# Performance work log

Measured on AMD Instinct MI355X. Metric: run time of the kernel, lower is better.

## Reference

```python
import jax, jax.numpy as jnp
import numpy as np

T, H, E, I, TOPK = 2048, 1024, 8, 2048, 2


def setup_inputs() -> dict:
    key = jax.random.key(0)
    k1, k2, k3, k4 = jax.random.split(key, 4)
    hidden_states = jax.random.normal(k1, (T, H), dtype=jnp.float32)
    router_logits = jax.random.normal(k2, (T, E), dtype=jnp.float32)
    # w13: merged gate+up projection [E, 2I, H]; w2: down projection [E, H, I]
    w13_weight = jax.random.normal(k3, (E, 2 * I, H), dtype=jnp.float32) * 0.02
    w2_weight = jax.random.normal(k4, (E, H, I), dtype=jnp.float32) * 0.02
    return {
        "hidden_states": hidden_states,
        "router_logits": router_logits,
        "w13_weight": w13_weight,
        "w2_weight": w2_weight,
        "top_k": TOPK,
    }


def reference(hidden_states, router_logits, w13_weight, w2_weight, top_k):
    num_experts = router_logits.shape[-1]
    # --- top-k routing (softmax -> top_k -> renormalize) ---
    probs = jax.nn.softmax(router_logits, axis=-1)           # [T, E]
    topk_w, topk_ids = jax.lax.top_k(probs, top_k)           # [T, K]
    topk_w = topk_w / jnp.sum(topk_w, axis=-1, keepdims=True)
    # per-token combine weight for each expert: [T, E]
    onehot = jax.nn.one_hot(topk_ids, num_experts, dtype=hidden_states.dtype)  # [T, K, E]
    combine_w = jnp.einsum("tk,tke->te", topk_w, onehot)
    # --- grouped expert GEMMs (gated SiLU MLP) ---
    gu = jnp.einsum("th,eih->tei", hidden_states, w13_weight)  # [T, E, 2I]
    inter = w13_weight.shape[1] // 2
    gate, up = gu[..., :inter], gu[..., inter:]
    act = jax.nn.silu(gate) * up                               # [T, E, I]
    y = jnp.einsum("tei,ehi->teh", act, w2_weight)             # [T, E, H]
    # --- combine ---
    out = jnp.einsum("teh,te->th", y, combine_w)               # [T, H]
    return out
```

## Files before the change

kernel.cpp:

```cpp
#include <hip/hip_runtime.h>

#define T_ 2048
#define H_ 1024
#define E_ 8
#define I_ 2048

typedef short bf16x8 __attribute__((ext_vector_type(8)));
typedef float f32x4 __attribute__((ext_vector_type(4)));
typedef unsigned short u16x8 __attribute__((ext_vector_type(8)));

__device__ __forceinline__ unsigned short f2bf(float f) {
  unsigned u = __builtin_bit_cast(unsigned, f);
  u += 0x7fffu + ((u >> 16) & 1u);
  return (unsigned short)(u >> 16);
}

__device__ __forceinline__ float bf2f(unsigned short h) {
  unsigned u = ((unsigned)h) << 16;
  return __builtin_bit_cast(float, u);
}

#define GLOAD_LDS16(g, l)                                                     \
  __builtin_amdgcn_global_load_lds(                                           \
      (const __attribute__((address_space(1))) unsigned int*)(g),             \
      (__attribute__((address_space(3))) unsigned int*)(l), 16, 0, 0)

__global__ __launch_bounds__(256) void cvt_kernel(const float* __restrict__ s,
                                                  unsigned short* __restrict__ d,
                                                  int n8) {
  int i = blockIdx.x * blockDim.x + threadIdx.x;
  if (i >= n8) return;
  const float4* s4 = (const float4*)s;
  float4 a = s4[2 * i], b = s4[2 * i + 1];
  u16x8 v;
  v[0] = f2bf(a.x); v[1] = f2bf(a.y); v[2] = f2bf(a.z); v[3] = f2bf(a.w);
  v[4] = f2bf(b.x); v[5] = f2bf(b.y); v[6] = f2bf(b.z); v[7] = f2bf(b.w);
  *(u16x8*)(d + (size_t)i * 8) = v;
}

__global__ __launch_bounds__(256) void pack_w13(const float* __restrict__ src,
                                                unsigned short* __restrict__ dst) {
  int g = blockIdx.x * 256 + threadIdx.x;
#pragma unroll
  for (int j = 0; j < 4; ++j) {
    size_t fo = ((size_t)g * 4 + j) * 8;
    int e = (int)(fo >> 22);
    int grow = (int)((fo >> 10) & 4095);
    int col = (int)(fo & 1023);
    int nt, r;
    if (grow < 2048) { nt = grow >> 6; r = grow & 63; }
    else             { int i2 = grow - 2048; nt = i2 >> 6; r = 64 + (i2 & 63); }
    int kt = col >> 6;
    int c = (col & 63) >> 3;
    const float4* s = (const float4*)(src + fo);
    float4 a = s[0], b = s[1];
    u16x8 o;
    o[0] = f2bf(a.x); o[1] = f2bf(a.y); o[2] = f2bf(a.z); o[3] = f2bf(a.w);
    o[4] = f2bf(b.x); o[5] = f2bf(b.y); o[6] = f2bf(b.z); o[7] = f2bf(b.w);
    size_t tb = (size_t)((e * 32 + nt) * 16 + kt);
    *(u16x8*)(dst + tb * 8192 + r * 64 + ((c ^ (r & 7)) * 8)) = o;
  }
}

__global__ __launch_bounds__(256) void pack_w2(const float* __restrict__ src,
                                               unsigned short* __restrict__ dst) {
  int g = blockIdx.x * 256 + threadIdx.x;
#pragma unroll
  for (int j = 0; j < 4; ++j) {
    size_t fo = ((size_t)g * 4 + j) * 8;
    int e = (int)(fo >> 21);
    int h = (int)((fo >> 11) & 1023);
    int col = (int)(fo & 2047);
    int nt = h >> 7, r = h & 127;
    int kt = col >> 6;
    int c = (col & 63) >> 3;
    const float4* s = (const float4*)(src + fo);
    float4 a = s[0], b = s[1];
    u16x8 o;
    o[0] = f2bf(a.x); o[1] = f2bf(a.y); o[2] = f2bf(a.z); o[3] = f2bf(a.w);
    o[4] = f2bf(b.x); o[5] = f2bf(b.y); o[6] = f2bf(b.z); o[7] = f2bf(b.w);
    size_t tb = (size_t)((e * 8 + nt) * 32 + kt);
    *(u16x8*)(dst + tb * 8192 + r * 64 + ((c ^ (r & 7)) * 8)) = o;
  }
}

__global__ void router_kernel(const float* __restrict__ logits,
                              int* __restrict__ cnt,
                              int* __restrict__ plist,
                              float* __restrict__ wlist) {
  int t = blockIdx.x * blockDim.x + threadIdx.x;
  if (t >= T_) return;
  float l[E_];
#pragma unroll
  for (int e = 0; e < E_; ++e) l[e] = logits[t * E_ + e];
  int i0 = 0;
#pragma unroll
  for (int e = 1; e < E_; ++e) if (l[e] > l[i0]) i0 = e;
  int i1 = (i0 == 0) ? 1 : 0;
#pragma unroll
  for (int e = 0; e < E_; ++e) if (e != i0 && l[e] > l[i1]) i1 = e;
  float w1 = 1.f / (1.f + __expf(l[i0] - l[i1]));
  float w0 = 1.f - w1;
  int s0 = atomicAdd(&cnt[i0], 1);
  plist[i0 * T_ + s0] = 2 * t;
  wlist[i0 * T_ + s0] = w0;
  int s1 = atomicAdd(&cnt[i1], 1);
  plist[i1 * T_ + s1] = 2 * t + 1;
  wlist[i1 * T_ + s1] = w1;
}

__global__ __launch_bounds__(512, 4) void gemm1_kernel(
    const unsigned short* __restrict__ hs_bf,
    const unsigned short* __restrict__ w13p,
    const int* __restrict__ cnt, const int* __restrict__ plist,
    const float* __restrict__ wlist, unsigned short* __restrict__ act) {
  const int bid = blockIdx.x;
  const int e = bid & 7;
  const int mt = (bid >> 3) & 15;
  const int nt = bid >> 7;
  const int M = cnt[e];
  if (mt * 128 >= M) return;
  const int Mrem = M - mt * 128;
  const int n0 = nt * 64;

  __shared__ __align__(16) unsigned short As[2][128 * 64];
  __shared__ __align__(16) unsigned short Bs[2][128 * 64];

  const int tid = threadIdx.x;
  const int lane = tid & 63;
  const int wid = tid >> 6;
  const int l15 = lane & 15;
  const int q = lane >> 4;
  const int wm = (wid >> 1) * 32;
  const int wn = (wid & 1) * 32;

  const unsigned short* aSrc[2];
#pragma unroll
  for (int i = 0; i < 2; ++i) {
    int row = wid * 16 + i * 8 + (lane >> 3);
    int idx = mt * 128 + ((row < Mrem) ? row : 0);
    int p = plist[e * T_ + idx] >> 1;
    aSrc[i] = hs_bf + (size_t)p * H_ + ((lane & 7) ^ (row & 7)) * 8;
  }
  const unsigned short* bTile = w13p + (size_t)((e * 32 + nt) * 16) * 8192;

#define STAGE_G1(buf, kt)                                                     \
  do {                                                                        \
    _Pragma("unroll") for (int i = 0; i < 2; ++i)                             \
        GLOAD_LDS16(aSrc[i] + (kt) * 64, &As[buf][(wid * 16 + i * 8) * 64]);  \
    _Pragma("unroll") for (int i = 0; i < 2; ++i)                             \
        GLOAD_LDS16(bTile + (size_t)(kt) * 8192 + (wid * 2 + i) * 512 +       \
                        lane * 8,                                             \
                    &Bs[buf][(wid * 2 + i) * 512]);                           \
  } while (0)

  f32x4 accg[2][2] = {};
  f32x4 accu[2][2] = {};

  STAGE_G1(0, 0);
#pragma unroll 1
  for (int kt = 0; kt < 16; ++kt) {
    const int buf = kt & 1;
    if (kt + 1 < 16) {
      STAGE_G1(buf ^ 1, kt + 1);
      asm volatile("s_waitcnt vmcnt(4)" ::: "memory");
    } else {
      asm volatile("s_waitcnt vmcnt(0)" ::: "memory");
    }
    __builtin_amdgcn_s_barrier();
    __builtin_amdgcn_sched_barrier(0);
#pragma unroll
    for (int ks = 0; ks < 2; ++ks) {
      const int co = ((ks * 4 + q) ^ (l15 & 7)) * 8;
      bf16x8 a0 = *(const bf16x8*)&As[buf][(wm + l15) * 64 + co];
      bf16x8 a1 = *(const bf16x8*)&As[buf][(wm + 16 + l15) * 64 + co];
      bf16x8 g0 = *(const bf16x8*)&Bs[buf][(wn + l15) * 64 + co];
      bf16x8 g1 = *(const bf16x8*)&Bs[buf][(wn + 16 + l15) * 64 + co];
      bf16x8 u0 = *(const bf16x8*)&Bs[buf][(64 + wn + l15) * 64 + co];
      bf16x8 u1 = *(const bf16x8*)&Bs[buf][(64 + wn + 16 + l15) * 64 + co];
      accg[0][0] = __builtin_amdgcn_mfma_f32_16x16x32_bf16(a0, g0, accg[0][0], 0, 0, 0);
      accg[0][1] = __builtin_amdgcn_mfma_f32_16x16x32_bf16(a0, g1, accg[0][1], 0, 0, 0);
      accg[1][0] = __builtin_amdgcn_mfma_f32_16x16x32_bf16(a1, g0, accg[1][0], 0, 0, 0);
      accg[1][1] = __builtin_amdgcn_mfma_f32_16x16x32_bf16(a1, g1, accg[1][1], 0, 0, 0);
      accu[0][0] = __builtin_amdgcn_mfma_f32_16x16x32_bf16(a0, u0, accu[0][0], 0, 0, 0);
      accu[0][1] = __builtin_amdgcn_mfma_f32_16x16x32_bf16(a0, u1, accu[0][1], 0, 0, 0);
      accu[1][0] = __builtin_amdgcn_mfma_f32_16x16x32_bf16(a1, u0, accu[1][0], 0, 0, 0);
      accu[1][1] = __builtin_amdgcn_mfma_f32_16x16x32_bf16(a1, u1, accu[1][1], 0, 0, 0);
    }
    __builtin_amdgcn_sched_barrier(0);
    __builtin_amdgcn_s_barrier();
  }

#pragma unroll
  for (int mi = 0; mi < 2; ++mi) {
#pragma unroll
    for (int rr = 0; rr < 4; ++rr) {
      int rl = wm + mi * 16 + q * 4 + rr;
      if (rl < Mrem) {
        int idx = mt * 128 + rl;
        int p = plist[e * T_ + idx];
        float w = wlist[e * T_ + idx];
        unsigned short* dst = act + (size_t)p * I_ + n0;
#pragma unroll
        for (int ni = 0; ni < 2; ++ni) {
          float g = accg[mi][ni][rr];
          float u = accu[mi][ni][rr];
          float a = (g / (1.f + __expf(-g))) * u * w;
          dst[wn + ni * 16 + l15] = f2bf(a);
        }
      }
    }
  }
}

__global__ __launch_bounds__(512, 4) void gemm2_kernel(
    const unsigned short* __restrict__ act,
    const unsigned short* __restrict__ w2p,
    const int* __restrict__ cnt, const int* __restrict__ plist,
    unsigned short* __restrict__ part) {
  const int bid = blockIdx.x;
  const int e = bid & 7;
  const int mt = (bid >> 3) & 15;
  const int nt = (bid >> 7) & 7;
  const int kb = bid >> 10;
  const int M = cnt[e];
  if (mt * 128 >= M) return;
  const int Mrem = M - mt * 128;
  const int n0 = nt * 128;
  const int k0 = kb * 1024;

  __shared__ __align__(16) unsigned short As[2][128 * 64];
  __shared__ __align__(16) unsigned short Bs[2][128 * 64];

  const int tid = threadIdx.x;
  const int lane = tid & 63;
  const int wid = tid >> 6;
  const int l15 = lane & 15;
  const int q = lane >> 4;
  const int wm = (wid >> 1) * 32;
  const int wn = (wid & 1) * 64;

  const unsigned short* aSrc[2];
#pragma unroll
  for (int i = 0; i < 2; ++i) {
    int row = wid * 16 + i * 8 + (lane >> 3);
    int idx = mt * 128 + ((row < Mrem) ? row : 0);
    int p = plist[e * T_ + idx];
    aSrc[i] = act + (size_t)p * I_ + k0 + ((lane & 7) ^ (row & 7)) * 8;
  }
  const unsigned short* bTile = w2p + (size_t)((e * 8 + nt) * 32 + kb * 16) * 8192;

#define STAGE_G2(buf, kt)                                                     \
  do {                                                                        \
    _Pragma("unroll") for (int i = 0; i < 2; ++i)                             \
        GLOAD_LDS16(aSrc[i] + (kt) * 64, &As[buf][(wid * 16 + i * 8) * 64]);  \
    _Pragma("unroll") for (int i = 0; i < 2; ++i)                             \
        GLOAD_LDS16(bTile + (size_t)(kt) * 8192 + (wid * 2 + i) * 512 +       \
                        lane * 8,                                             \
                    &Bs[buf][(wid * 2 + i) * 512]);                           \
  } while (0)

  f32x4 acc[2][4] = {};

  STAGE_G2(0, 0);
#pragma unroll 1
  for (int kt = 0; kt < 16; ++kt) {
    const int buf = kt & 1;
    if (kt + 1 < 16) {
      STAGE_G2(buf ^ 1, kt + 1);
      asm volatile("s_waitcnt vmcnt(4)" ::: "memory");
    } else {
      asm volatile("s_waitcnt vmcnt(0)" ::: "memory");
    }
    __builtin_amdgcn_s_barrier();
    __builtin_amdgcn_sched_barrier(0);
#pragma unroll
    for (int ks = 0; ks < 2; ++ks) {
      const int co = ((ks * 4 + q) ^ (l15 & 7)) * 8;
      bf16x8 a0 = *(const bf16x8*)&As[buf][(wm + l15) * 64 + co];
      bf16x8 a1 = *(const bf16x8*)&As[buf][(wm + 16 + l15) * 64 + co];
      bf16x8 b0 = *(const bf16x8*)&Bs[buf][(wn + l15) * 64 + co];
      bf16x8 b1 = *(const bf16x8*)&Bs[buf][(wn + 16 + l15) * 64 + co];
      bf16x8 b2 = *(const bf16x8*)&Bs[buf][(wn + 32 + l15) * 64 + co];
      bf16x8 b3 = *(const bf16x8*)&Bs[buf][(wn + 48 + l15) * 64 + co];
      acc[0][0] = __builtin_amdgcn_mfma_f32_16x16x32_bf16(a0, b0, acc[0][0], 0, 0, 0);
      acc[0][1] = __builtin_amdgcn_mfma_f32_16x16x32_bf16(a0, b1, acc[0][1], 0, 0, 0);
      acc[0][2] = __builtin_amdgcn_mfma_f32_16x16x32_bf16(a0, b2, acc[0][2], 0, 0, 0);
      acc[0][3] = __builtin_amdgcn_mfma_f32_16x16x32_bf16(a0, b3, acc[0][3], 0, 0, 0);
      acc[1][0] = __builtin_amdgcn_mfma_f32_16x16x32_bf16(a1, b0, acc[1][0], 0, 0, 0);
      acc[1][1] = __builtin_amdgcn_mfma_f32_16x16x32_bf16(a1, b1, acc[1][1], 0, 0, 0);
      acc[1][2] = __builtin_amdgcn_mfma_f32_16x16x32_bf16(a1, b2, acc[1][2], 0, 0, 0);
      acc[1][3] = __builtin_amdgcn_mfma_f32_16x16x32_bf16(a1, b3, acc[1][3], 0, 0, 0);
    }
    __builtin_amdgcn_sched_barrier(0);
    __builtin_amdgcn_s_barrier();
  }

#pragma unroll
  for (int mi = 0; mi < 2; ++mi) {
#pragma unroll
    for (int rr = 0; rr < 4; ++rr) {
      int rl = wm + mi * 16 + q * 4 + rr;
      if (rl < Mrem) {
        int p = plist[e * T_ + mt * 128 + rl];
        unsigned short* dst = part + ((size_t)kb * 2 * T_ + p) * H_ + n0 + wn + l15;
#pragma unroll
        for (int ni = 0; ni < 4; ++ni)
          dst[ni * 16] = f2bf(acc[mi][ni][rr]);
      }
    }
  }
}

__global__ __launch_bounds__(256) void reduce_kernel(const unsigned short* __restrict__ part,
                                                     float* __restrict__ out) {
  int i = blockIdx.x * blockDim.x + threadIdx.x;
  int t = i >> 7;
  int c = (i & 127) << 3;
  float s[8] = {0.f, 0.f, 0.f, 0.f, 0.f, 0.f, 0.f, 0.f};
#pragma unroll
  for (int kb = 0; kb < 2; ++kb) {
#pragma unroll
    for (int pp = 0; pp < 2; ++pp) {
      u16x8 v = *(const u16x8*)(part + ((size_t)kb * 2 * T_ + 2 * t + pp) * H_ + c);
#pragma unroll
      for (int j = 0; j < 8; ++j) s[j] += bf2f(v[j]);
    }
  }
  float* o = out + (size_t)t * H_ + c;
  *(f32x4*)o = *(f32x4*)&s[0];
  *(f32x4*)(o + 4) = *(f32x4*)&s[4];
}

extern "C" void kernel_launch(void* const* d_in, const int* in_sizes, int n_in,
                              void* d_out, int out_size, void* d_ws, size_t ws_size,
                              hipStream_t stream) {
  const float* hs     = (const float*)d_in[0];
  const float* logits = (const float*)d_in[1];
  const float* w13    = (const float*)d_in[2];
  const float* w2     = (const float*)d_in[3];
  float* out = (float*)d_out;

  char* ws = (char*)d_ws;
  size_t off = 0;
  int* cnt = (int*)(ws + off);           off += 256;
  int* plist = (int*)(ws + off);         off += (size_t)E_ * T_ * 4;
  float* wlist = (float*)(ws + off);     off += (size_t)E_ * T_ * 4;
  unsigned short* act = (unsigned short*)(ws + off);   off += (size_t)2 * T_ * I_ * 2;
  unsigned short* hs_bf = (unsigned short*)(ws + off); off += (size_t)T_ * H_ * 2;
  unsigned short* part = (unsigned short*)(ws + off);  off += (size_t)2 * 2 * T_ * H_ * 2;
  unsigned short* w13p = (unsigned short*)(ws + off);  off += (size_t)E_ * 2 * I_ * H_ * 2;
  unsigned short* w2p = (unsigned short*)(ws + off);   off += (size_t)E_ * H_ * I_ * 2;

  hipMemsetAsync(cnt, 0, 256, stream);

  const int nHs = T_ * H_ / 8;
  cvt_kernel<<<(nHs + 255) / 256, 256, 0, stream>>>(hs, hs_bf, nHs);
  router_kernel<<<T_ / 256, 256, 0, stream>>>(logits, cnt, plist, wlist);
  pack_w13<<<4096, 256, 0, stream>>>(w13, w13p);
  pack_w2<<<2048, 256, 0, stream>>>(w2, w2p);

  gemm1_kernel<<<32 * 16 * 8, 512, 0, stream>>>(hs_bf, w13p, cnt, plist, wlist, act);
  gemm2_kernel<<<2 * 8 * 16 * 8, 512, 0, stream>>>(act, w2p, cnt, plist, part);
  reduce_kernel<<<T_ * H_ / 8 / 256, 256, 0, stream>>>(part, out);
}
```

Measured before the change: 222.2 us.

## Use BK=32 tiles with triple-buffered LDS pipeline in both expert GEMMs

Halves the K-tile depth from 64 to 32 and repacks the bf16 weight layout to match (4-chunk XOR swizzle). Both GEMMs switch from double to triple buffering with a prefetch distance of two tiles, and occupancy hints rise from 4 to 6 blocks per CU, since the smaller LDS footprint should allow more resident blocks. The aim is better latency hiding of global-to-LDS loads. The cost is twice as many barriers per K step and less MFMA work between syncs.

```diff
diff --git a/kernel.cpp b/kernel.cpp
--- a/kernel.cpp
+++ b/kernel.cpp
@@ -50,15 +50,15 @@
     int nt, r;
     if (grow < 2048) { nt = grow >> 6; r = grow & 63; }
     else             { int i2 = grow - 2048; nt = i2 >> 6; r = 64 + (i2 & 63); }
-    int kt = col >> 6;
-    int c = (col & 63) >> 3;
+    int kt = col >> 5;
+    int c = (col & 31) >> 3;
     const float4* s = (const float4*)(src + fo);
     float4 a = s[0], b = s[1];
     u16x8 o;
     o[0] = f2bf(a.x); o[1] = f2bf(a.y); o[2] = f2bf(a.z); o[3] = f2bf(a.w);
     o[4] = f2bf(b.x); o[5] = f2bf(b.y); o[6] = f2bf(b.z); o[7] = f2bf(b.w);
-    size_t tb = (size_t)((e * 32 + nt) * 16 + kt);
-    *(u16x8*)(dst + tb * 8192 + r * 64 + ((c ^ (r & 7)) * 8)) = o;
+    size_t tb = (size_t)((e * 32 + nt) * 32 + kt);
+    *(u16x8*)(dst + tb * 4096 + r * 32 + ((c ^ (r & 3)) * 8)) = o;
   }
 }
 
@@ -72,15 +72,15 @@
     int h = (int)((fo >> 11) & 1023);
     int col = (int)(fo & 2047);
     int nt = h >> 7, r = h & 127;
-    int kt = col >> 6;
-    int c = (col & 63) >> 3;
+    int kt = col >> 5;
+    int c = (col & 31) >> 3;
     const float4* s = (const float4*)(src + fo);
     float4 a = s[0], b = s[1];
     u16x8 o;
     o[0] = f2bf(a.x); o[1] = f2bf(a.y); o[2] = f2bf(a.z); o[3] = f2bf(a.w);
     o[4] = f2bf(b.x); o[5] = f2bf(b.y); o[6] = f2bf(b.z); o[7] = f2bf(b.w);
-    size_t tb = (size_t)((e * 8 + nt) * 32 + kt);
-    *(u16x8*)(dst + tb * 8192 + r * 64 + ((c ^ (r & 7)) * 8)) = o;
+    size_t tb = (size_t)((e * 8 + nt) * 64 + kt);
+    *(u16x8*)(dst + tb * 4096 + r * 32 + ((c ^ (r & 3)) * 8)) = o;
   }
 }
 
@@ -109,7 +109,7 @@
   wlist[i1 * T_ + s1] = w1;
 }
 
-__global__ __launch_bounds__(512, 4) void gemm1_kernel(
+__global__ __launch_bounds__(512, 6) void gemm1_kernel(
     const unsigned short* __restrict__ hs_bf,
     const unsigned short* __restrict__ w13p,
     const int* __restrict__ cnt, const int* __restrict__ plist,
@@ -123,8 +123,8 @@
   const int Mrem = M - mt * 128;
   const int n0 = nt * 64;
 
-  __shared__ __align__(16) unsigned short As[2][128 * 64];
-  __shared__ __align__(16) unsigned short Bs[2][128 * 64];
+  __shared__ __align__(16) unsigned short As[3][128 * 32];
+  __shared__ __align__(16) unsigned short Bs[3][128 * 32];
 
   const int tid = threadIdx.x;
   const int lane = tid & 63;
@@ -134,59 +134,61 @@
   const int wm = (wid >> 1) * 32;
   const int wn = (wid & 1) * 32;
 
-  const unsigned short* aSrc[2];
-#pragma unroll
-  for (int i = 0; i < 2; ++i) {
-    int row = wid * 16 + i * 8 + (lane >> 3);
+  const unsigned short* aSrc;
+  {
+    int row = wid * 16 + (lane >> 2);
     int idx = mt * 128 + ((row < Mrem) ? row : 0);
     int p = plist[e * T_ + idx] >> 1;
-    aSrc[i] = hs_bf + (size_t)p * H_ + ((lane & 7) ^ (row & 7)) * 8;
-  }
-  const unsigned short* bTile = w13p + (size_t)((e * 32 + nt) * 16) * 8192;
+    aSrc = hs_bf + (size_t)p * H_ + ((lane & 3) ^ (row & 3)) * 8;
+  }
+  const unsigned short* bSrc;
+  {
+    int row = wid * 16 + (lane >> 2);
+    bSrc = w13p + (size_t)((e * 32 + nt) * 32) * 4096 + row * 32 + (lane & 3) * 8;
+  }
 
 #define STAGE_G1(buf, kt)                                                     \
   do {                                                                        \
-    _Pragma("unroll") for (int i = 0; i < 2; ++i)                             \
-        GLOAD_LDS16(aSrc[i] + (kt) * 64, &As[buf][(wid * 16 + i * 8) * 64]);  \
-    _Pragma("unroll") for (int i = 0; i < 2; ++i)                             \
-        GLOAD_LDS16(bTile + (size_t)(kt) * 8192 + (wid * 2 + i) * 512 +       \
-                        lane * 8,                                             \
-                    &Bs[buf][(wid * 2 + i) * 512]);                           \
+    GLOAD_LDS16(aSrc + (kt) * 32, &As[buf][(wid * 16) * 32]);                 \
+    GLOAD_LDS16(bSrc + (size_t)(kt) * 4096, &Bs[buf][(wid * 16) * 32]);       \
   } while (0)
 
   f32x4 accg[2][2] = {};
   f32x4 accu[2][2] = {};
 
   STAGE_G1(0, 0);
+  STAGE_G1(1, 1);
+
 #pragma unroll 1
-  for (int kt = 0; kt < 16; ++kt) {
-    const int buf = kt & 1;
-    if (kt + 1 < 16) {
-      STAGE_G1(buf ^ 1, kt + 1);
+  for (int kt = 0; kt < 32; ++kt) {
+    const int buf = kt % 3;
+    if (kt + 2 < 32) {
+      STAGE_G1((kt + 2) % 3, kt + 2);
       asm volatile("s_waitcnt vmcnt(4)" ::: "memory");
+    } else if (kt + 1 < 32) {
+      asm volatile("s_waitcnt vmcnt(2)" ::: "memory");
     } else {
       asm volatile("s_waitcnt vmcnt(0)" ::: "memory");
     }
     __builtin_amdgcn_s_barrier();
     __builtin_amdgcn_sched_barrier(0);
-#pragma unroll
-    for (int ks = 0; ks < 2; ++ks) {
-      const int co = ((ks * 4 + q) ^ (l15 & 7)) * 8;
-      bf16x8 a0 = *(const bf16x8*)&As[buf][(wm + l15) * 64 + co];
-      bf16x8 a1 = *(const bf16x8*)&As[buf][(wm + 16 + l15) * 64 + co];
-      bf16x8 g0 = *(const bf16x8*)&Bs[buf][(wn + l15) * 64 + co];
-      bf16x8 g1 = *(const bf16x8*)&Bs[buf][(wn + 16 + l15) * 64 + co];
-      bf16x8 u0 = *(const bf16x8*)&Bs[buf][(64 + wn + l15) * 64 + co];
-      bf16x8 u1 = *(const bf16x8*)&Bs[buf][(64 + wn + 16 + l15) * 64 + co];
-      accg[0][0] = __builtin_amdgcn_mfma_f32_16x16x32_bf16(a0, g0, accg[0][0], 0, 0, 0);
-      accg[0][1] = __builtin_amdgcn_mfma_f32_16x16x32_bf16(a0, g1, accg[0][1], 0, 0, 0);
-      accg[1][0] = __builtin_amdgcn_mfma_f32_16x16x32_bf16(a1, g0, accg[1][0], 0, 0, 0);
-      accg[1][1] = __builtin_amdgcn_mfma_f32_16x16x32_bf16(a1, g1, accg[1][1], 0, 0, 0);
-      accu[0][0] = __builtin_amdgcn_mfma_f32_16x16x32_bf16(a0, u0, accu[0][0], 0, 0, 0);
-      accu[0][1] = __builtin_amdgcn_mfma_f32_16x16x32_bf16(a0, u1, accu[0][1], 0, 0, 0);
-      accu[1][0] = __builtin_amdgcn_mfma_f32_16x16x32_bf16(a1, u0, accu[1][0], 0, 0, 0);
-      accu[1][1] = __builtin_amdgcn_mfma_f32_16x16x32_bf16(a1, u1, accu[1][1], 0, 0, 0);
-    }
+
+    const int co = (q ^ (l15 & 3)) * 8;
+    bf16x8 a0 = *(const bf16x8*)&As[buf][(wm + l15) * 32 + co];
+    bf16x8 a1 = *(const bf16x8*)&As[buf][(wm + 16 + l15) * 32 + co];
+    bf16x8 g0 = *(const bf16x8*)&Bs[buf][(wn + l15) * 32 + co];
+    bf16x8 g1 = *(const bf16x8*)&Bs[buf][(wn + 16 + l15) * 32 + co];
+    bf16x8 u0 = *(const bf16x8*)&Bs[buf][(64 + wn + l15) * 32 + co];
+    bf16x8 u1 = *(const bf16x8*)&Bs[buf][(64 + wn + 16 + l15) * 32 + co];
+    accg[0][0] = __builtin_amdgcn_mfma_f32_16x16x32_bf16(a0, g0, accg[0][0], 0, 0, 0);
+    accg[0][1] = __builtin_amdgcn_mfma_f32_16x16x32_bf16(a0, g1, accg[0][1], 0, 0, 0);
+    accg[1][0] = __builtin_amdgcn_mfma_f32_16x16x32_bf16(a1, g0, accg[1][0], 0, 0, 0);
+    accg[1][1] = __builtin_amdgcn_mfma_f32_16x16x32_bf16(a1, g1, accg[1][1], 0, 0, 0);
+    accu[0][0] = __builtin_amdgcn_mfma_f32_16x16x32_bf16(a0, u0, accu[0][0], 0, 0, 0);
+    accu[0][1] = __builtin_amdgcn_mfma_f32_16x16x32_bf16(a0, u1, accu[0][1], 0, 0, 0);
+    accu[1][0] = __builtin_amdgcn_mfma_f32_16x16x32_bf16(a1, u0, accu[1][0], 0, 0, 0);
+    accu[1][1] = __builtin_amdgcn_mfma_f32_16x16x32_bf16(a1, u1, accu[1][1], 0, 0, 0);
+
     __builtin_amdgcn_sched_barrier(0);
     __builtin_amdgcn_s_barrier();
   }
@@ -213,7 +215,7 @@
   }
 }
 
-__global__ __launch_bounds__(512, 4) void gemm2_kernel(
+__global__ __launch_bounds__(512, 6) void gemm2_kernel(
     const unsigned short* __restrict__ act,
     const unsigned short* __restrict__ w2p,
     const int* __restrict__ cnt, const int* __restrict__ plist,
@@ -229,8 +231,8 @@
   const int n0 = nt * 128;
   const int k0 = kb * 1024;
 
-  __shared__ __align__(16) unsigned short As[2][128 * 64];
-  __shared__ __align__(16) unsigned short Bs[2][128 * 64];
+  __shared__ __align__(16) unsigned short As[3][128 * 32];
+  __shared__ __align__(16) unsigned short Bs[3][128 * 32];
 
   const int tid = threadIdx.x;
   const int lane = tid & 63;
@@ -240,58 +242,60 @@
   const int wm = (wid >> 1) * 32;
   const int wn = (wid & 1) * 64;
 
-  const unsigned short* aSrc[2];
-#pragma unroll
-  for (int i = 0; i < 2; ++i) {
-    int row = wid * 16 + i * 8 + (lane >> 3);
+  const unsigned short* aSrc;
+  {
+    int row = wid * 16 + (lane >> 2);
     int idx = mt * 128 + ((row < Mrem) ? row : 0);
     int p = plist[e * T_ + idx];
-    aSrc[i] = act + (size_t)p * I_ + k0 + ((lane & 7) ^ (row & 7)) * 8;
-  }
-  const unsigned short* bTile = w2p + (size_t)((e * 8 + nt) * 32 + kb * 16) * 8192;
+    aSrc = act + (size_t)p * I_ + k0 + ((lane & 3) ^ (row & 3)) * 8;
+  }
+  const unsigned short* bSrc;
+  {
+    int row = wid * 16 + (lane >> 2);
+    bSrc = w2p + (size_t)((e * 8 + nt) * 64 + kb * 32) * 4096 + row * 32 + (lane & 3) * 8;
+  }
 
 #define STAGE_G2(buf, kt)                                                     \
   do {                                                                        \
-    _Pragma("unroll") for (int i = 0; i < 2; ++i)                             \
-        GLOAD_LDS16(aSrc[i] + (kt) * 64, &As[buf][(wid * 16 + i * 8) * 64]);  \
-    _Pragma("unroll") for (int i = 0; i < 2; ++i)                             \
-        GLOAD_LDS16(bTile + (size_t)(kt) * 8192 + (wid * 2 + i) * 512 +       \
-                        lane * 8,                                             \
-                    &Bs[buf][(wid * 2 + i) * 512]);                           \
+    GLOAD_LDS16(aSrc + (kt) * 32, &As[buf][(wid * 16) * 32]);                 \
+    GLOAD_LDS16(bSrc + (size_t)(kt) * 4096, &Bs[buf][(wid * 16) * 32]);       \
   } while (0)
 
   f32x4 acc[2][4] = {};
 
   STAGE_G2(0, 0);
+  STAGE_G2(1, 1);
+
 #pragma unroll 1
-  for (int kt = 0; kt < 16; ++kt) {
-    const int buf = kt & 1;
-    if (kt + 1 < 16) {
-      STAGE_G2(buf ^ 1, kt + 1);
+  for (int kt = 0; kt < 32; ++kt) {
+    const int buf = kt % 3;
+    if (kt + 2 < 32) {
+      STAGE_G2((kt + 2) % 3, kt + 2);
       asm volatile("s_waitcnt vmcnt(4)" ::: "memory");
+    } else if (kt + 1 < 32) {
+      asm volatile("s_waitcnt vmcnt(2)" ::: "memory");
     } else {
       asm volatile("s_waitcnt vmcnt(0)" ::: "memory");
     }
     __builtin_amdgcn_s_barrier();
     __builtin_amdgcn_sched_barrier(0);
-#pragma unroll
-    for (int ks = 0; ks < 2; ++ks) {
-      const int co = ((ks * 4 + q) ^ (l15 & 7)) * 8;
-      bf16x8 a0 = *(const bf16x8*)&As[buf][(wm + l15) * 64 + co];
-      bf16x8 a1 = *(const bf16x8*)&As[buf][(wm + 16 + l15) * 64 + co];
-      bf16x8 b0 = *(const bf16x8*)&Bs[buf][(wn + l15) * 64 + co];
-      bf16x8 b1 = *(const bf16x8*)&Bs[buf][(wn + 16 + l15) * 64 + co];
-      bf16x8 b2 = *(const bf16x8*)&Bs[buf][(wn + 32 + l15) * 64 + co];
-      bf16x8 b3 = *(const bf16x8*)&Bs[buf][(wn + 48 + l15) * 64 + co];
-      acc[0][0] = __builtin_amdgcn_mfma_f32_16x16x32_bf16(a0, b0, acc[0][0], 0, 0, 0);
-      acc[0][1] = __builtin_amdgcn_mfma_f32_16x16x32_bf16(a0, b1, acc[0][1], 0, 0, 0);
-      acc[0][2] = __builtin_amdgcn_mfma_f32_16x16x32_bf16(a0, b2, acc[0][2], 0, 0, 0);
-      acc[0][3] = __builtin_amdgcn_mfma_f32_16x16x32_bf16(a0, b3, acc[0][3], 0, 0, 0);
-      acc[1][0] = __builtin_amdgcn_mfma_f32_16x16x32_bf16(a1, b0, acc[1][0], 0, 0, 0);
-      acc[1][1] = __builtin_amdgcn_mfma_f32_16x16x32_bf16(a1, b1, acc[1][1], 0, 0, 0);
-      acc[1][2] = __builtin_amdgcn_mfma_f32_16x16x32_bf16(a1, b2, acc[1][2], 0, 0, 0);
-      acc[1][3] = __builtin_amdgcn_mfma_f32_16x16x32_bf16(a1, b3, acc[1][3], 0, 0, 0);
-    }
+
+    const int co = (q ^ (l15 & 3)) * 8;
+    bf16x8 a0 = *(const bf16x8*)&As[buf][(wm + l15) * 32 + co];
+    bf16x8 a1 = *(const bf16x8*)&As[buf][(wm + 16 + l15) * 32 + co];
+    bf16x8 b0 = *(const bf16x8*)&Bs[buf][(wn + l15) * 32 + co];
+    bf16x8 b1 = *(const bf16x8*)&Bs[buf][(wn + 16 + l15) * 32 + co];
+    bf16x8 b2 = *(const bf16x8*)&Bs[buf][(wn + 32 + l15) * 32 + co];
+    bf16x8 b3 = *(const bf16x8*)&Bs[buf][(wn + 48 + l15) * 32 + co];
+    acc[0][0] = __builtin_amdgcn_mfma_f32_16x16x32_bf16(a0, b0, acc[0][0], 0, 0, 0);
+    acc[0][1] = __builtin_amdgcn_mfma_f32_16x16x32_bf16(a0, b1, acc[0][1], 0, 0, 0);
+    acc[0][2] = __builtin_amdgcn_mfma_f32_16x16x32_bf16(a0, b2, acc[0][2], 0, 0, 0);
+    acc[0][3] = __builtin_amdgcn_mfma_f32_16x16x32_bf16(a0, b3, acc[0][3], 0, 0, 0);
+    acc[1][0] = __builtin_amdgcn_mfma_f32_16x16x32_bf16(a1, b0, acc[1][0], 0, 0, 0);
+    acc[1][1] = __builtin_amdgcn_mfma_f32_16x16x32_bf16(a1, b1, acc[1][1], 0, 0, 0);
+    acc[1][2] = __builtin_amdgcn_mfma_f32_16x16x32_bf16(a1, b2, acc[1][2], 0, 0, 0);
+    acc[1][3] = __builtin_amdgcn_mfma_f32_16x16x32_bf16(a1, b3, acc[1][3], 0, 0, 0);
+
     __builtin_amdgcn_sched_barrier(0);
     __builtin_amdgcn_s_barrier();
   }
```

New measurement: 231.6 us. 4.2% more time.
